# Kernel optimization log

Hardware: AMD Instinct MI355X
Metric: run time of the kernel (lower is better)

The kernel has to match this reference:

```python
import jax, jax.numpy as jnp
import numpy as np

B, S, IN, OUT, P = 4, 1024, 128, 128, 16
CTX = min(IN, OUT)
MAX_SEQ = 4096


def setup_inputs() -> dict:
    key = jax.random.key(0)
    keys = iter(jax.random.split(key, 32))
    nk = lambda: next(keys)

    def linear(fi, fo):
        lim = 1.0 / np.sqrt(fi)
        W = jax.random.uniform(nk(), (fi, fo), jnp.float32, -lim, lim)
        b = jax.random.uniform(nk(), (fo,), jnp.float32, -lim, lim)
        return W, b

    x = jax.random.normal(nk(), (B, S, IN), jnp.float32)
    context_features = jax.random.normal(nk(), (B, S, CTX), jnp.float32)
    flow_patterns = jax.random.normal(nk(), (P, OUT, IN), jnp.float32) * 0.1
    w_sel1, b_sel1 = linear(IN + CTX, 2 * P)
    w_sel2, b_sel2 = linear(2 * P, P)
    w_int1, b_int1 = linear(IN + CTX, 64)
    w_int2, b_int2 = linear(64, 1)
    w_win1, b_win1 = linear(IN, 64)
    w_win2, b_win2 = linear(64, 1)
    return dict(x=x, context_features=context_features, flow_patterns=flow_patterns,
                w_sel1=w_sel1, b_sel1=b_sel1, w_sel2=w_sel2, b_sel2=b_sel2,
                w_int1=w_int1, b_int1=b_int1, w_int2=w_int2, b_int2=b_int2,
                w_win1=w_win1, b_win1=b_win1, w_win2=w_win2, b_win2=b_win2)


def _gelu(v):
    return jax.nn.gelu(v, approximate=False)  # torch nn.GELU default (erf)


def reference(x, context_features, flow_patterns,
              w_sel1, b_sel1, w_sel2, b_sel2,
              w_int1, b_int1, w_int2, b_int2,
              w_win1, b_win1, w_win2, b_win2):
    # combined input [B,S,IN+CTX]
    combined = jnp.concatenate([x, context_features], axis=-1)
    # pattern weights [B,S,P]
    pattern_weights = jax.nn.softmax(_gelu(combined @ w_sel1 + b_sel1) @ w_sel2 + b_sel2, axis=-1)
    # per-token flow matrix [B,S,OUT,IN]
    flow = jnp.einsum('bsp,poi->bsoi', pattern_weights, flow_patterns)
    # flow intensity [B,S,1] -> [B,S,1,1]
    intensity = jax.nn.sigmoid(_gelu(combined @ w_int1 + b_int1) @ w_int2 + b_int2)
    flow = flow * intensity[..., None]
    # adaptive window size [B,1]
    window_size = jax.nn.sigmoid(_gelu(x.mean(axis=1) @ w_win1 + b_win1) @ w_win2 + b_win2)
    window_size = window_size * (MAX_SEQ - 256) + 256
    # context-aware topk sparsity over flattened out*in dim
    adaptive_sparsity = 0.1 * jnp.mean(window_size / MAX_SEQ)  # scalar
    D = OUT * IN
    k = jnp.maximum(1, jnp.floor(D * adaptive_sparsity)).astype(jnp.int32)
    flat = flow.reshape(B, S, D)
    a = jnp.abs(flat)
    sorted_a = jnp.sort(a, axis=-1)  # ascending
    # k-th largest abs value per (b,s) row; k is a traced scalar -> dynamic_slice
    thr = jax.lax.dynamic_slice_in_dim(sorted_a, D - k, 1, axis=-1)  # [B,S,1]
    mask = jax.lax.stop_gradient((a >= thr).astype(flat.dtype))
    return (mask * flat).reshape(B, S, OUT, IN)
```

## Files before the change

### kernel.cpp

```cpp
#include <hip/hip_runtime.h>
#include <math.h>

#define S_   1024
#define D_   16384
#define CAPA 192
#define CAPL 256

typedef float v4f __attribute__((ext_vector_type(4)));

__device__ __forceinline__ double gelu64(double v) {
    return 0.5 * v * (1.0 + erf(v * 0.70710678118654752440));
}
__device__ __forceinline__ double sigmoid64(double z) {
    return 1.0 / (1.0 + exp(-z));
}

__global__ __launch_bounds__(256) void mlp_kernel(
    const float* __restrict__ x, const float* __restrict__ ctx,
    const float* __restrict__ w_sel1, const float* __restrict__ b_sel1,
    const float* __restrict__ w_sel2, const float* __restrict__ b_sel2,
    const float* __restrict__ w_int1, const float* __restrict__ b_int1,
    const float* __restrict__ w_int2, const float* __restrict__ b_int2,
    double* __restrict__ pw64, float* __restrict__ pw32,
    double* __restrict__ it64, float* __restrict__ it32)
{
    __shared__ double comb[4][256];
    __shared__ double hpart[2][4][32];
    __shared__ double h1[4][32];
    const int tid = threadIdx.x;
    const int tok0 = blockIdx.x * 4;

    for (int r = 0; r < 4; ++r) {
        int idx = tid + r * 256;
        int t = idx >> 8, i = idx & 255;
        comb[t][i] = (double)((i < 128) ? x[(tok0 + t) * 128 + i]
                                        : ctx[(tok0 + t) * 128 + (i - 128)]);
    }
    __syncthreads();

    {
        int u = tid & 31, t = (tid >> 5) & 3, half = tid >> 7;
        int i0 = half * 128;
        double s0 = (half == 0) ? (double)b_sel1[u] : 0.0, s1 = 0.0;
        for (int i = 0; i < 128; i += 2) {
            s0 = fma(comb[t][i0 + i],     (double)w_sel1[(i0 + i) * 32 + u],     s0);
            s1 = fma(comb[t][i0 + i + 1], (double)w_sel1[(i0 + i + 1) * 32 + u], s1);
        }
        hpart[half][t][u] = s0 + s1;
    }
    __syncthreads();
    if (tid < 128) {
        int t = tid >> 5, u = tid & 31;
        h1[t][u] = gelu64(hpart[0][t][u] + hpart[1][t][u]);
    }
    __syncthreads();
    if (tid < 64) {
        int t = tid >> 4, u = tid & 15;
        double z = (double)b_sel2[u];
        for (int j = 0; j < 32; ++j)
            z = fma(h1[t][j], (double)w_sel2[j * 16 + u], z);
        double m = z;
        for (int off = 8; off >= 1; off >>= 1) m = fmax(m, __shfl_xor(m, off));
        double e = exp(z - m);
        double ssum = e;
        for (int off = 8; off >= 1; off >>= 1) ssum += __shfl_xor(ssum, off);
        double pwv = e / ssum;
        pw64[(tok0 + t) * 16 + u] = pwv;
        pw32[(tok0 + t) * 16 + u] = (float)pwv;
    }
    {
        int t = tid >> 6, u = tid & 63;
        double a0 = (double)b_int1[u], a1 = 0.0, a2 = 0.0, a3 = 0.0;
        for (int i = 0; i < 256; i += 4) {
            a0 = fma(comb[t][i],     (double)w_int1[i * 64 + u],       a0);
            a1 = fma(comb[t][i + 1], (double)w_int1[(i + 1) * 64 + u], a1);
            a2 = fma(comb[t][i + 2], (double)w_int1[(i + 2) * 64 + u], a2);
            a3 = fma(comb[t][i + 3], (double)w_int1[(i + 3) * 64 + u], a3);
        }
        double c = gelu64((a0 + a1) + (a2 + a3)) * (double)w_int2[u];
        for (int off = 32; off >= 1; off >>= 1) c += __shfl_xor(c, off);
        if (u == 0) {
            double iv = sigmoid64(c + (double)b_int2[0]);
            it64[tok0 + t] = iv;
            it32[tok0 + t] = (float)iv;
        }
    }
}

__global__ __launch_bounds__(256) void win_part_kernel(
    const float* __restrict__ x, double* __restrict__ wpart)
{
    __shared__ double red[2][128];
    const int tid = threadIdx.x;
    const int b = blockIdx.x >> 4, chunk = blockIdx.x & 15;
    int i = tid & 127, h = tid >> 7;
    double a0 = 0.0, a1 = 0.0;
    int s0 = b * S_ + chunk * 64 + h * 32;
    for (int j = 0; j < 32; j += 2) {
        a0 += (double)x[(s0 + j) * 128 + i];
        a1 += (double)x[(s0 + j + 1) * 128 + i];
    }
    red[h][i] = a0 + a1;
    __syncthreads();
    if (tid < 128)
        wpart[(b * 16 + chunk) * 128 + tid] = red[0][tid] + red[1][tid];
}

__global__ __launch_bounds__(256) void win_fin_kernel(
    const double* __restrict__ wpart,
    const float* __restrict__ w_win1, const float* __restrict__ b_win1,
    const float* __restrict__ w_win2, const float* __restrict__ b_win2,
    double* __restrict__ win_out)
{
    __shared__ double xm[4][128];
    const int tid = threadIdx.x;
    const int b = tid >> 6, lane = tid & 63;
    for (int r = 0; r < 2; ++r) {
        int i = lane + r * 64;
        double s = 0.0;
        for (int c = 0; c < 16; ++c)
            s += wpart[(b * 16 + c) * 128 + i];
        xm[b][i] = s * (1.0 / 1024.0);
    }
    __syncthreads();
    {
        int u = lane;
        double s0 = (double)b_win1[u], s1 = 0.0;
        for (int i = 0; i < 128; i += 2) {
            s0 = fma(xm[b][i],     (double)w_win1[i * 64 + u],       s0);
            s1 = fma(xm[b][i + 1], (double)w_win1[(i + 1) * 64 + u], s1);
        }
        double c = gelu64(s0 + s1) * (double)w_win2[u];
        for (int off = 32; off >= 1; off >>= 1) c += __shfl_xor(c, off);
        if (lane == 0)
            win_out[b] = sigmoid64(c + (double)b_win2[0]) * 3840.0 + 256.0;
    }
}

__global__ __launch_bounds__(256, 3) void flow_kernel(
    const float* __restrict__ patterns,
    const double* __restrict__ pw64, const float* __restrict__ pw32,
    const double* __restrict__ it64, const float* __restrict__ it32,
    const double* __restrict__ win,
    float* __restrict__ out)
{
    __shared__ int sred[2][4];
    __shared__ float smax[2][4];
    __shared__ unsigned listIdx[2][CAPL];
    __shared__ double listVal[2][CAPL];
    __shared__ unsigned flagBits[2][512];
    __shared__ unsigned listCnt[2];

    const int tid = threadIdx.x;
    const int lane = tid & 63, wv = tid >> 6;
    const int t0 = blockIdx.x * 2, t1 = t0 + 1;

    if (tid < 2) listCnt[tid] = 0;
    for (int r = tid; r < 1024; r += 256) flagBits[r >> 9][r & 511] = 0;

    double w0 = win[0] * (1.0 / 4096.0), w1 = win[1] * (1.0 / 4096.0);
    double w2 = win[2] * (1.0 / 4096.0), w3 = win[3] * (1.0 / 4096.0);
    double mean = (((w0 + w1) + w2) + w3) * 0.25;
    double kd = floor(16384.0 * (0.1 * mean));
    int k = (kd < 1.0) ? 1 : (int)kd;

    float qw0[16], qw1[16];
#pragma unroll
    for (int p = 0; p < 16; ++p) {
        qw0[p] = pw32[t0 * 16 + p];
        qw1[p] = pw32[t1 * 16 + p];
    }
    float i0 = it32[t0], i1 = it32[t1];

    const v4f* pat4 = (const v4f*)patterns;
    v4f v0[16], v1[16];
#pragma unroll
    for (int c = 0; c < 16; ++c) {
        int grp = c * 256 + tid;
        v4f a0 = (v4f)(0.0f), a1 = (v4f)(0.0f);
#pragma unroll
        for (int p = 0; p < 16; ++p) {
            v4f pp = pat4[p * 4096 + grp];
            a0 += qw0[p] * pp;
            a1 += qw1[p] * pp;
        }
        v0[c] = a0 * i0;
        v1[c] = a1 * i1;
    }

    float mx0 = 0.0f, mx1 = 0.0f;
#pragma unroll
    for (int c = 0; c < 16; ++c) {
        mx0 = fmaxf(mx0, fmaxf(fmaxf(fabsf(v0[c].x), fabsf(v0[c].y)),
                               fmaxf(fabsf(v0[c].z), fabsf(v0[c].w))));
        mx1 = fmaxf(mx1, fmaxf(fmaxf(fabsf(v1[c].x), fabsf(v1[c].y)),
                               fmaxf(fabsf(v1[c].z), fabsf(v1[c].w))));
    }
    for (int off = 32; off >= 1; off >>= 1) {
        mx0 = fmaxf(mx0, __shfl_xor(mx0, off));
        mx1 = fmaxf(mx1, __shfl_xor(mx1, off));
    }
    if (lane == 0) { smax[0][wv] = mx0; smax[1][wv] = mx1; }
    __syncthreads();
    mx0 = fmaxf(fmaxf(smax[0][0], smax[0][1]), fmaxf(smax[0][2], smax[0][3]));
    mx1 = fmaxf(fmaxf(smax[1][0], smax[1][1]), fmaxf(smax[1][2], smax[1][3]));

    unsigned lo0 = 0, hi0 = __float_as_uint(mx0) + 1;
    unsigned lo1 = 0, hi1 = __float_as_uint(mx1) + 1;
    int clo0 = D_, chi0 = 0, clo1 = D_, chi1 = 0;
    int par = 0;
    while (((clo0 - chi0 > CAPA) && (hi0 - lo0 > 1)) ||
           ((clo1 - chi1 > CAPA) && (hi1 - lo1 > 1))) {
        unsigned c0k = (lo0 + hi0) >> 1, c1k = (lo1 + hi1) >> 1;
        float c0 = __uint_as_float(c0k), c1 = __uint_as_float(c1k);
        int n0 = 0, n1 = 0;
#pragma unroll
        for (int c = 0; c < 16; ++c) {
            n0 += (fabsf(v0[c].x) >= c0); n0 += (fabsf(v0[c].y) >= c0);
            n0 += (fabsf(v0[c].z) >= c0); n0 += (fabsf(v0[c].w) >= c0);
            n1 += (fabsf(v1[c].x) >= c1); n1 += (fabsf(v1[c].y) >= c1);
            n1 += (fabsf(v1[c].z) >= c1); n1 += (fabsf(v1[c].w) >= c1);
        }
        int pk = n0 | (n1 << 16);
#pragma unroll
        for (int off = 32; off >= 1; off >>= 1) pk += __shfl_xor(pk, off);
        if (lane == 0) sred[par][wv] = pk;
        __syncthreads();
        int tot = sred[par][0] + sred[par][1] + sred[par][2] + sred[par][3];
        par ^= 1;
        int tc0 = tot & 0xffff, tc1 = tot >> 16;
        if (hi0 - lo0 > 1) { if (tc0 >= k) { lo0 = c0k; clo0 = tc0; } else { hi0 = c0k; chi0 = tc0; } }
        if (hi1 - lo1 > 1) { if (tc1 >= k) { lo1 = c1k; clo1 = tc1; } else { hi1 = c1k; chi1 = tc1; } }
    }

    float E0 = 3e-6f * i0, E1 = 3e-6f * i1;
    float loCut0 = __uint_as_float(lo0) - 2.0f * E0, hiCut0 = __uint_as_float(hi0) + 2.0f * E0;
    float loCut1 = __uint_as_float(lo1) - 2.0f * E1, hiCut1 = __uint_as_float(hi1) + 2.0f * E1;

    int ns0 = 0, ns1 = 0;
#pragma unroll
    for (int c = 0; c < 16; ++c) {
#pragma unroll
        for (int q = 0; q < 4; ++q) {
            unsigned e = (unsigned)(4 * (c * 256 + tid) + q);
            float a0 = fabsf(v0[c][q]);
            if (a0 >= hiCut0) ns0++;
            else if (a0 >= loCut0) {
                unsigned pos = atomicAdd(&listCnt[0], 1u);
                if (pos < CAPL) listIdx[0][pos] = e;
            }
            float a1 = fabsf(v1[c][q]);
            if (a1 >= hiCut1) ns1++;
            else if (a1 >= loCut1) {
                unsigned pos = atomicAdd(&listCnt[1], 1u);
                if (pos < CAPL) listIdx[1][pos] = e;
            }
        }
    }
    {
        int pk = ns0 | (ns1 << 16);
#pragma unroll
        for (int off = 32; off >= 1; off >>= 1) pk += __shfl_xor(pk, off);
        if (lane == 0) sred[par][wv] = pk;
    }
    __syncthreads();
    int tot = sred[par][0] + sred[par][1] + sred[par][2] + sred[par][3];
    int m0 = k - (tot & 0xffff), m1 = k - (tot >> 16);
    int c0n = (int)(listCnt[0] < CAPL ? listCnt[0] : CAPL);
    int c1n = (int)(listCnt[1] < CAPL ? listCnt[1] : CAPL);

    double itt0 = it64[t0], itt1 = it64[t1];
    int totL = c0n + c1n;
    for (int g = tid; g < totL; g += 256) {
        int tk = (g >= c0n);
        int e = tk ? (g - c0n) : g;
        unsigned idx = listIdx[tk][e];
        const double* pwp = pw64 + (tk ? t1 : t0) * 16;
        double s = 0.0;
#pragma unroll
        for (int p = 0; p < 16; ++p)
            s = fma(pwp[p], (double)patterns[p * D_ + idx], s);
        listVal[tk][e] = fabs(s * (tk ? itt1 : itt0));
    }
    __syncthreads();
    for (int g = tid; g < totL; g += 256) {
        int tk = (g >= c0n);
        int e = tk ? (g - c0n) : g;
        double my = listVal[tk][e];
        int cnt = tk ? c1n : c0n, m = tk ? m1 : m0;
        int r = 0;
        for (int j = 0; j < cnt; ++j) r += (listVal[tk][j] > my);
        if (r < m) {
            unsigned idx = listIdx[tk][e];
            atomicOr(&flagBits[tk][idx >> 5], 1u << (idx & 31));
        }
    }
    __syncthreads();

    v4f* o0p = (v4f*)(out + (size_t)t0 * D_);
    v4f* o1p = (v4f*)(out + (size_t)t1 * D_);
#pragma unroll
    for (int c = 0; c < 16; ++c) {
        int grp = c * 256 + tid;
        v4f r0, r1;
#pragma unroll
        for (int q = 0; q < 4; ++q) {
            unsigned e = (unsigned)(4 * grp + q);
            float av = fabsf(v0[c][q]);
            bool keep = (av >= hiCut0);
            if (!keep && av >= loCut0) keep = (flagBits[0][e >> 5] >> (e & 31)) & 1u;
            r0[q] = keep ? v0[c][q] : 0.0f;
            av = fabsf(v1[c][q]);
            keep = (av >= hiCut1);
            if (!keep && av >= loCut1) keep = (flagBits[1][e >> 5] >> (e & 31)) & 1u;
            r1[q] = keep ? v1[c][q] : 0.0f;
        }
        __builtin_nontemporal_store(r0, &o0p[grp]);
        __builtin_nontemporal_store(r1, &o1p[grp]);
    }
}

extern "C" void kernel_launch(void* const* d_in, const int* in_sizes, int n_in,
                              void* d_out, int out_size, void* d_ws, size_t ws_size,
                              hipStream_t stream) {
    const float* x        = (const float*)d_in[0];
    const float* ctx      = (const float*)d_in[1];
    const float* patterns = (const float*)d_in[2];
    const float* w_sel1   = (const float*)d_in[3];
    const float* b_sel1   = (const float*)d_in[4];
    const float* w_sel2   = (const float*)d_in[5];
    const float* b_sel2   = (const float*)d_in[6];
    const float* w_int1   = (const float*)d_in[7];
    const float* b_int1   = (const float*)d_in[8];
    const float* w_int2   = (const float*)d_in[9];
    const float* b_int2   = (const float*)d_in[10];
    const float* w_win1   = (const float*)d_in[11];
    const float* b_win1   = (const float*)d_in[12];
    const float* w_win2   = (const float*)d_in[13];
    const float* b_win2   = (const float*)d_in[14];

    double* ws    = (double*)d_ws;
    double* win   = ws;
    double* pw64  = ws + 8;
    double* it64  = pw64 + 65536;
    double* wpart = it64 + 4096;
    float*  pw32  = (float*)(wpart + 8192);
    float*  it32  = pw32 + 65536;
    float*  out   = (float*)d_out;

    hipLaunchKernelGGL(mlp_kernel, dim3(1024), dim3(256), 0, stream,
                       x, ctx, w_sel1, b_sel1, w_sel2, b_sel2,
                       w_int1, b_int1, w_int2, b_int2, pw64, pw32, it64, it32);
    hipLaunchKernelGGL(win_part_kernel, dim3(64), dim3(256), 0, stream, x, wpart);
    hipLaunchKernelGGL(win_fin_kernel, dim3(1), dim3(256), 0, stream,
                       wpart, w_win1, b_win1, w_win2, b_win2, win);
    hipLaunchKernelGGL(flow_kernel, dim3(2048), dim3(256), 0, stream,
                       patterns, pw64, pw32, it64, it32, win, out);
}
```

Measured before the change: 516.2 us.

## Replace bisection threshold search with shared-memory histogram and widen flow blocks

The top-k threshold search no longer bisects over float bits with repeated block-wide count reductions. It builds a 512-bin histogram of exponent/mantissa-prefix buckets in shared memory with atomics, then finds the bucket containing the k-th largest value using a wave-level suffix scan. The candidate list capacity doubles to absorb the wider bucket. The flow kernel moves to 512 threads per block with half the register tiles per thread, and the MLP kernel is split to 2 tokens per block using shuffle reductions. The trade-off is shared-atomic contention and possibly more candidates to rank exactly, which could overflow the list cap.

```diff
diff --git a/kernel.cpp b/kernel.cpp
--- a/kernel.cpp
+++ b/kernel.cpp
@@ -3,8 +3,8 @@
 
 #define S_   1024
 #define D_   16384
-#define CAPA 192
-#define CAPL 256
+#define CAPL 512
+#define NB   512
 
 typedef float v4f __attribute__((ext_vector_type(4)));
 
@@ -13,6 +13,9 @@
 }
 __device__ __forceinline__ double sigmoid64(double z) {
     return 1.0 / (1.0 + exp(-z));
+}
+__device__ __forceinline__ float rfl(float x) {
+    return __uint_as_float(__builtin_amdgcn_readfirstlane(__float_as_uint(x)));
 }
 
 __global__ __launch_bounds__(256) void mlp_kernel(
@@ -24,66 +27,72 @@
     double* __restrict__ pw64, float* __restrict__ pw32,
     double* __restrict__ it64, float* __restrict__ it32)
 {
-    __shared__ double comb[4][256];
-    __shared__ double hpart[2][4][32];
-    __shared__ double h1[4][32];
+    __shared__ double comb[2][256];
+    __shared__ double h1[2][32];
+    __shared__ double ipart[2][2];
     const int tid = threadIdx.x;
-    const int tok0 = blockIdx.x * 4;
-
-    for (int r = 0; r < 4; ++r) {
+    const int tok0 = blockIdx.x * 2;
+    const int t = tid >> 7, local = tid & 127;
+
+    for (int r = 0; r < 2; ++r) {
         int idx = tid + r * 256;
-        int t = idx >> 8, i = idx & 255;
-        comb[t][i] = (double)((i < 128) ? x[(tok0 + t) * 128 + i]
-                                        : ctx[(tok0 + t) * 128 + (i - 128)]);
+        int tk = idx >> 8, i = idx & 255;
+        comb[tk][i] = (double)((i < 128) ? x[(tok0 + tk) * 128 + i]
+                                         : ctx[(tok0 + tk) * 128 + (i - 128)]);
     }
     __syncthreads();
 
     {
-        int u = tid & 31, t = (tid >> 5) & 3, half = tid >> 7;
-        int i0 = half * 128;
-        double s0 = (half == 0) ? (double)b_sel1[u] : 0.0, s1 = 0.0;
-        for (int i = 0; i < 128; i += 2) {
+        int u = local >> 2, sl = local & 3;
+        int i0 = sl * 64;
+        double s0 = (sl == 0) ? (double)b_sel1[u] : 0.0, s1 = 0.0;
+        for (int i = 0; i < 64; i += 2) {
             s0 = fma(comb[t][i0 + i],     (double)w_sel1[(i0 + i) * 32 + u],     s0);
             s1 = fma(comb[t][i0 + i + 1], (double)w_sel1[(i0 + i + 1) * 32 + u], s1);
         }
-        hpart[half][t][u] = s0 + s1;
-    }
-    __syncthreads();
-    if (tid < 128) {
-        int t = tid >> 5, u = tid & 31;
-        h1[t][u] = gelu64(hpart[0][t][u] + hpart[1][t][u]);
-    }
-    __syncthreads();
-    if (tid < 64) {
-        int t = tid >> 4, u = tid & 15;
+        double s = s0 + s1;
+        s += __shfl_xor(s, 1);
+        s += __shfl_xor(s, 2);
+        if (sl == 0) h1[t][u] = gelu64(s);
+    }
+    {
+        int u = local >> 1, sl = local & 1;
+        int i0 = sl * 128;
+        double a0 = (sl == 0) ? (double)b_int1[u] : 0.0, a1 = 0.0, a2 = 0.0, a3 = 0.0;
+        for (int i = 0; i < 128; i += 4) {
+            a0 = fma(comb[t][i0 + i],     (double)w_int1[(i0 + i) * 64 + u],     a0);
+            a1 = fma(comb[t][i0 + i + 1], (double)w_int1[(i0 + i + 1) * 64 + u], a1);
+            a2 = fma(comb[t][i0 + i + 2], (double)w_int1[(i0 + i + 2) * 64 + u], a2);
+            a3 = fma(comb[t][i0 + i + 3], (double)w_int1[(i0 + i + 3) * 64 + u], a3);
+        }
+        double s = (a0 + a1) + (a2 + a3);
+        s += __shfl_xor(s, 1);
+        double val = (sl == 0) ? gelu64(s) * (double)w_int2[u] : 0.0;
+        for (int off = 2; off <= 32; off <<= 1)
+            val += __shfl_xor(val, off);
+        val += __shfl_xor(val, 1);
+        if ((local & 63) == 0) ipart[t][local >> 6] = val;
+    }
+    __syncthreads();
+
+    if (tid < 32) {
+        int t2 = tid >> 4, u = tid & 15;
         double z = (double)b_sel2[u];
         for (int j = 0; j < 32; ++j)
-            z = fma(h1[t][j], (double)w_sel2[j * 16 + u], z);
+            z = fma(h1[t2][j], (double)w_sel2[j * 16 + u], z);
         double m = z;
         for (int off = 8; off >= 1; off >>= 1) m = fmax(m, __shfl_xor(m, off));
         double e = exp(z - m);
         double ssum = e;
         for (int off = 8; off >= 1; off >>= 1) ssum += __shfl_xor(ssum, off);
         double pwv = e / ssum;
-        pw64[(tok0 + t) * 16 + u] = pwv;
-        pw32[(tok0 + t) * 16 + u] = (float)pwv;
-    }
-    {
-        int t = tid >> 6, u = tid & 63;
-        double a0 = (double)b_int1[u], a1 = 0.0, a2 = 0.0, a3 = 0.0;
-        for (int i = 0; i < 256; i += 4) {
-            a0 = fma(comb[t][i],     (double)w_int1[i * 64 + u],       a0);
-            a1 = fma(comb[t][i + 1], (double)w_int1[(i + 1) * 64 + u], a1);
-            a2 = fma(comb[t][i + 2], (double)w_int1[(i + 2) * 64 + u], a2);
-            a3 = fma(comb[t][i + 3], (double)w_int1[(i + 3) * 64 + u], a3);
-        }
-        double c = gelu64((a0 + a1) + (a2 + a3)) * (double)w_int2[u];
-        for (int off = 32; off >= 1; off >>= 1) c += __shfl_xor(c, off);
-        if (u == 0) {
-            double iv = sigmoid64(c + (double)b_int2[0]);
-            it64[tok0 + t] = iv;
-            it32[tok0 + t] = (float)iv;
-        }
+        pw64[(tok0 + t2) * 16 + u] = pwv;
+        pw32[(tok0 + t2) * 16 + u] = (float)pwv;
+    } else if (tid < 34) {
+        int t3 = tid - 32;
+        double iv = sigmoid64(ipart[t3][0] + ipart[t3][1] + (double)b_int2[0]);
+        it64[tok0 + t3] = iv;
+        it32[tok0 + t3] = (float)iv;
     }
 }
 
@@ -137,26 +146,29 @@
     }
 }
 
-__global__ __launch_bounds__(256, 3) void flow_kernel(
+__global__ __launch_bounds__(512, 4) void flow_kernel(
     const float* __restrict__ patterns,
     const double* __restrict__ pw64, const float* __restrict__ pw32,
     const double* __restrict__ it64, const float* __restrict__ it32,
     const double* __restrict__ win,
     float* __restrict__ out)
 {
-    __shared__ int sred[2][4];
-    __shared__ float smax[2][4];
+    __shared__ unsigned hist[2][NB];
+    __shared__ unsigned flagBits[2][512];
     __shared__ unsigned listIdx[2][CAPL];
     __shared__ double listVal[2][CAPL];
-    __shared__ unsigned flagBits[2][512];
+    __shared__ float smax[2][8];
+    __shared__ int sred[8];
+    __shared__ int bcastB[2];
     __shared__ unsigned listCnt[2];
 
     const int tid = threadIdx.x;
     const int lane = tid & 63, wv = tid >> 6;
     const int t0 = blockIdx.x * 2, t1 = t0 + 1;
 
+    for (int r = tid; r < 2 * NB; r += 512) hist[r >> 9][r & (NB - 1)] = 0;
+    for (int r = tid; r < 1024; r += 512) flagBits[r >> 9][r & 511] = 0;
     if (tid < 2) listCnt[tid] = 0;
-    for (int r = tid; r < 1024; r += 256) flagBits[r >> 9][r & 511] = 0;
 
     double w0 = win[0] * (1.0 / 4096.0), w1 = win[1] * (1.0 / 4096.0);
     double w2 = win[2] * (1.0 / 4096.0), w3 = win[3] * (1.0 / 4096.0);
@@ -167,16 +179,16 @@
     float qw0[16], qw1[16];
 #pragma unroll
     for (int p = 0; p < 16; ++p) {
-        qw0[p] = pw32[t0 * 16 + p];
-        qw1[p] = pw32[t1 * 16 + p];
-    }
-    float i0 = it32[t0], i1 = it32[t1];
+        qw0[p] = rfl(pw32[t0 * 16 + p]);
+        qw1[p] = rfl(pw32[t1 * 16 + p]);
+    }
+    float i0 = rfl(it32[t0]), i1 = rfl(it32[t1]);
 
     const v4f* pat4 = (const v4f*)patterns;
-    v4f v0[16], v1[16];
-#pragma unroll
-    for (int c = 0; c < 16; ++c) {
-        int grp = c * 256 + tid;
+    v4f v0[8], v1[8];
+#pragma unroll
+    for (int c = 0; c < 8; ++c) {
+        int grp = c * 512 + tid;
         v4f a0 = (v4f)(0.0f), a1 = (v4f)(0.0f);
 #pragma unroll
         for (int p = 0; p < 16; ++p) {
@@ -190,7 +202,7 @@
 
     float mx0 = 0.0f, mx1 = 0.0f;
 #pragma unroll
-    for (int c = 0; c < 16; ++c) {
+    for (int c = 0; c < 8; ++c) {
         mx0 = fmaxf(mx0, fmaxf(fmaxf(fabsf(v0[c].x), fabsf(v0[c].y)),
                                fmaxf(fabsf(v0[c].z), fabsf(v0[c].w))));
         mx1 = fmaxf(mx1, fmaxf(fmaxf(fabsf(v1[c].x), fabsf(v1[c].y)),
@@ -202,47 +214,70 @@
     }
     if (lane == 0) { smax[0][wv] = mx0; smax[1][wv] = mx1; }
     __syncthreads();
-    mx0 = fmaxf(fmaxf(smax[0][0], smax[0][1]), fmaxf(smax[0][2], smax[0][3]));
-    mx1 = fmaxf(fmaxf(smax[1][0], smax[1][1]), fmaxf(smax[1][2], smax[1][3]));
-
-    unsigned lo0 = 0, hi0 = __float_as_uint(mx0) + 1;
-    unsigned lo1 = 0, hi1 = __float_as_uint(mx1) + 1;
-    int clo0 = D_, chi0 = 0, clo1 = D_, chi1 = 0;
-    int par = 0;
-    while (((clo0 - chi0 > CAPA) && (hi0 - lo0 > 1)) ||
-           ((clo1 - chi1 > CAPA) && (hi1 - lo1 > 1))) {
-        unsigned c0k = (lo0 + hi0) >> 1, c1k = (lo1 + hi1) >> 1;
-        float c0 = __uint_as_float(c0k), c1 = __uint_as_float(c1k);
-        int n0 = 0, n1 = 0;
-#pragma unroll
-        for (int c = 0; c < 16; ++c) {
-            n0 += (fabsf(v0[c].x) >= c0); n0 += (fabsf(v0[c].y) >= c0);
-            n0 += (fabsf(v0[c].z) >= c0); n0 += (fabsf(v0[c].w) >= c0);
-            n1 += (fabsf(v1[c].x) >= c1); n1 += (fabsf(v1[c].y) >= c1);
-            n1 += (fabsf(v1[c].z) >= c1); n1 += (fabsf(v1[c].w) >= c1);
-        }
-        int pk = n0 | (n1 << 16);
-#pragma unroll
-        for (int off = 32; off >= 1; off >>= 1) pk += __shfl_xor(pk, off);
-        if (lane == 0) sred[par][wv] = pk;
-        __syncthreads();
-        int tot = sred[par][0] + sred[par][1] + sred[par][2] + sred[par][3];
-        par ^= 1;
-        int tc0 = tot & 0xffff, tc1 = tot >> 16;
-        if (hi0 - lo0 > 1) { if (tc0 >= k) { lo0 = c0k; clo0 = tc0; } else { hi0 = c0k; chi0 = tc0; } }
-        if (hi1 - lo1 > 1) { if (tc1 >= k) { lo1 = c1k; clo1 = tc1; } else { hi1 = c1k; chi1 = tc1; } }
-    }
+    mx0 = smax[0][0]; mx1 = smax[1][0];
+#pragma unroll
+    for (int w = 1; w < 8; ++w) {
+        mx0 = fmaxf(mx0, smax[0][w]);
+        mx1 = fmaxf(mx1, smax[1][w]);
+    }
+    int base0 = (int)(__float_as_uint(mx0) >> 17) - (NB - 1);
+    int base1 = (int)(__float_as_uint(mx1) >> 17) - (NB - 1);
+    if (base0 < 0) base0 = 0;
+    if (base1 < 0) base1 = 0;
+
+#pragma unroll
+    for (int c = 0; c < 8; ++c) {
+#pragma unroll
+        for (int q = 0; q < 4; ++q) {
+            int b0 = (int)(__float_as_uint(fabsf(v0[c][q])) >> 17) - base0;
+            if (b0 > 0) atomicAdd(&hist[0][b0 > NB - 1 ? NB - 1 : b0], 1u);
+            int b1 = (int)(__float_as_uint(fabsf(v1[c][q])) >> 17) - base1;
+            if (b1 > 0) atomicAdd(&hist[1][b1 > NB - 1 ? NB - 1 : b1], 1u);
+        }
+    }
+    __syncthreads();
+
+    if (wv < 2) {
+        int t = wv;
+        int sum8 = 0;
+#pragma unroll
+        for (int j = 0; j < 8; ++j) sum8 += (int)hist[t][lane * 8 + j];
+        int suffix = sum8;
+        for (int off = 1; off <= 32; off <<= 1) {
+            int other = __shfl_down(suffix, off);
+            if (lane + off < 64) suffix += other;
+        }
+        int sufNext = __shfl_down(suffix, 1);
+        if (lane == 63) sufNext = 0;
+        unsigned long long msk = __ballot(suffix >= k);
+        int Lstar = (msk == 0) ? 0 : (63 - __clzll(msk));
+        if (lane == Lstar) {
+            int cnt = sufNext, B = Lstar * 8;
+            for (int j = 7; j >= 0; --j) {
+                cnt += (int)hist[t][Lstar * 8 + j];
+                if (cnt >= k) { B = Lstar * 8 + j; break; }
+            }
+            bcastB[t] = B;
+        }
+    }
+    __syncthreads();
+
+    int B0 = bcastB[0], B1 = bcastB[1];
+    float loF0 = (B0 + base0) ? __uint_as_float((unsigned)(B0 + base0) << 17) : 0.0f;
+    float hiF0 = __uint_as_float((unsigned)(B0 + base0 + 1) << 17);
+    float loF1 = (B1 + base1) ? __uint_as_float((unsigned)(B1 + base1) << 17) : 0.0f;
+    float hiF1 = __uint_as_float((unsigned)(B1 + base1 + 1) << 17);
 
     float E0 = 3e-6f * i0, E1 = 3e-6f * i1;
-    float loCut0 = __uint_as_float(lo0) - 2.0f * E0, hiCut0 = __uint_as_float(hi0) + 2.0f * E0;
-    float loCut1 = __uint_as_float(lo1) - 2.0f * E1, hiCut1 = __uint_as_float(hi1) + 2.0f * E1;
+    float loCut0 = loF0 - 2.0f * E0, hiCut0 = hiF0 + 2.0f * E0;
+    float loCut1 = loF1 - 2.0f * E1, hiCut1 = hiF1 + 2.0f * E1;
 
     int ns0 = 0, ns1 = 0;
 #pragma unroll
-    for (int c = 0; c < 16; ++c) {
+    for (int c = 0; c < 8; ++c) {
 #pragma unroll
         for (int q = 0; q < 4; ++q) {
-            unsigned e = (unsigned)(4 * (c * 256 + tid) + q);
+            unsigned e = (unsigned)(4 * (c * 512 + tid) + q);
             float a0 = fabsf(v0[c][q]);
             if (a0 >= hiCut0) ns0++;
             else if (a0 >= loCut0) {
@@ -261,17 +296,19 @@
         int pk = ns0 | (ns1 << 16);
 #pragma unroll
         for (int off = 32; off >= 1; off >>= 1) pk += __shfl_xor(pk, off);
-        if (lane == 0) sred[par][wv] = pk;
-    }
-    __syncthreads();
-    int tot = sred[par][0] + sred[par][1] + sred[par][2] + sred[par][3];
+        if (lane == 0) sred[wv] = pk;
+    }
+    __syncthreads();
+    int tot = 0;
+#pragma unroll
+    for (int w = 0; w < 8; ++w) tot += sred[w];
     int m0 = k - (tot & 0xffff), m1 = k - (tot >> 16);
     int c0n = (int)(listCnt[0] < CAPL ? listCnt[0] : CAPL);
     int c1n = (int)(listCnt[1] < CAPL ? listCnt[1] : CAPL);
 
     double itt0 = it64[t0], itt1 = it64[t1];
     int totL = c0n + c1n;
-    for (int g = tid; g < totL; g += 256) {
+    for (int g = tid; g < totL; g += 512) {
         int tk = (g >= c0n);
         int e = tk ? (g - c0n) : g;
         unsigned idx = listIdx[tk][e];
@@ -283,7 +320,7 @@
         listVal[tk][e] = fabs(s * (tk ? itt1 : itt0));
     }
     __syncthreads();
-    for (int g = tid; g < totL; g += 256) {
+    for (int g = tid; g < totL; g += 512) {
         int tk = (g >= c0n);
         int e = tk ? (g - c0n) : g;
         double my = listVal[tk][e];
@@ -300,8 +337,8 @@
     v4f* o0p = (v4f*)(out + (size_t)t0 * D_);
     v4f* o1p = (v4f*)(out + (size_t)t1 * D_);
 #pragma unroll
-    for (int c = 0; c < 16; ++c) {
-        int grp = c * 256 + tid;
+    for (int c = 0; c < 8; ++c) {
+        int grp = c * 512 + tid;
         v4f r0, r1;
 #pragma unroll
         for (int q = 0; q < 4; ++q) {
@@ -348,12 +385,12 @@
     float*  it32  = pw32 + 65536;
     float*  out   = (float*)d_out;
 
-    hipLaunchKernelGGL(mlp_kernel, dim3(1024), dim3(256), 0, stream,
+    hipLaunchKernelGGL(mlp_kernel, dim3(2048), dim3(256), 0, stream,
                        x, ctx, w_sel1, b_sel1, w_sel2, b_sel2,
                        w_int1, b_int1, w_int2, b_int2, pw64, pw32, it64, it32);
     hipLaunchKernelGGL(win_part_kernel, dim3(64), dim3(256), 0, stream, x, wpart);
     hipLaunchKernelGGL(win_fin_kernel, dim3(1), dim3(256), 0, stream,
                        wpart, w_win1, b_win1, w_win2, b_win2, win);
-    hipLaunchKernelGGL(flow_kernel, dim3(2048), dim3(256), 0, stream,
+    hipLaunchKernelGGL(flow_kernel, dim3(2048), dim3(512), 0, stream,
                        patterns, pw64, pw32, it64, it32, win, out);
 }
```

Measured after the change: 445.2 us. -13.8%, faster.
